# Kernel tuning notes

Hardware: AMD Instinct MI355X
Metric: run time of the kernel (lower is better)

The kernel has to match this reference:

```python
import jax, jax.numpy as jnp
import numpy as np

B, N, DEG = 8, 4096, 16
E = N * DEG            # edges per graph
IN, HID, C, OUT = 128, 512, 2, 10
EPS = 1e-15


def setup_inputs() -> dict:
    key = jax.random.key(0)
    ks = jax.random.split(key, 16)
    # within-graph random edges, then offset each graph by b*N
    src = jax.random.randint(ks[0], (B, E), 0, N)
    dst = jax.random.randint(ks[1], (B, E), 0, N)
    off = (jnp.arange(B) * N)[:, None]
    edge_index = jnp.stack([(src + off).reshape(-1), (dst + off).reshape(-1)], axis=0).astype(jnp.int64)
    batch = jnp.repeat(jnp.arange(B), N).astype(jnp.int64)
    x = jax.random.normal(ks[2], (B * N, IN), dtype=jnp.float32)
    edge_weight = jax.random.uniform(ks[3], (B * E,), dtype=jnp.float32)
    g = lambda k, s: (0.02 * jax.random.normal(k, s, dtype=jnp.float32))
    return {
        "x": x, "edge_index": edge_index, "batch": batch, "edge_weight": edge_weight,
        "W_rel1": g(ks[4], (IN, HID)), "b_rel1": jnp.zeros((HID,), jnp.float32),
        "W_root1": g(ks[5], (IN, HID)),
        "W_pool": g(ks[6], (HID, C)), "b_pool": jnp.zeros((C,), jnp.float32),
        "W_rel3": g(ks[7], (HID, HID)), "b_rel3": jnp.zeros((HID,), jnp.float32),
        "W_root3": g(ks[8], (HID, HID)),
        "W_lin1": g(ks[9], (HID, HID)), "b_lin1": jnp.zeros((HID,), jnp.float32),
        "W_lin2": g(ks[10], (HID, OUT)), "b_lin2": jnp.zeros((OUT,), jnp.float32),
    }


def reference(x, edge_index, batch, edge_weight,
              W_rel1, b_rel1, W_root1, W_pool, b_pool,
              W_rel3, b_rel3, W_root3, W_lin1, b_lin1, W_lin2, b_lin2):
    src, dst = edge_index[0], edge_index[1]
    # GraphConv (aggr='add'): out = lin_rel(sum_j w_ji x_j) + lin_root(x)
    agg = jax.ops.segment_sum(x[src] * edge_weight[:, None], dst, num_segments=B * N)
    h = jax.nn.relu(agg @ W_rel1 + b_rel1 + x @ W_root1)          # [BN, HID]
    s_logits = h @ W_pool + b_pool                                 # [BN, C]

    # dense batched tensors (equal-size graphs)
    hd = h.reshape(B, N, HID)
    s = jax.nn.softmax(s_logits.reshape(B, N, C), axis=-1)
    b_idx = batch[src]
    r = src - b_idx * N
    c = dst - b_idx * N
    adj = jnp.zeros((B, N, N), jnp.float32).at[b_idx, r, c].add(edge_weight)

    # dense mincut pooling
    out = jnp.einsum('bnc,bnf->bcf', s, hd)                        # [B, C, HID]
    sA = jnp.einsum('bnc,bnm->bcm', s, adj)
    out_adj = jnp.einsum('bcm,bmk->bck', sA, s)                    # [B, C, C]
    mincut_num = jnp.einsum('bcc->b', out_adj)
    d = adj.sum(-1)                                                # [B, N]
    mincut_den = jnp.einsum('bnc,bn,bnc->b', s, d, s)
    mc_loss = jnp.mean(-(mincut_num / mincut_den))
    ss = jnp.einsum('bnc,bnk->bck', s, s)
    ss_n = ss / jnp.linalg.norm(ss, axis=(1, 2), keepdims=True)
    i_s = jnp.eye(C, dtype=jnp.float32) / jnp.sqrt(jnp.float32(C))
    o_loss = jnp.mean(jnp.linalg.norm(ss_n - i_s[None], axis=(1, 2)))
    # zero diagonal + symmetric degree normalization
    out_adj = out_adj * (1.0 - jnp.eye(C, dtype=jnp.float32))[None]
    d2 = jnp.sqrt(out_adj.sum(-1)) + EPS                           # [B, C]
    out_adj = out_adj / d2[:, :, None] / d2[:, None, :]

    # conv3 on pooled graph: edges (row->col) of dense adj => agg = A^T x
    agg3 = jnp.einsum('bij,bif->bjf', out_adj, out)
    x3 = agg3 @ W_rel3 + b_rel3 + out @ W_root3                    # [B, C, HID]
    xm = x3.mean(axis=1)                                           # [B, HID]
    h2 = jax.nn.relu(xm @ W_lin1 + b_lin1)
    logits = h2 @ W_lin2 + b_lin2
    return (jax.nn.log_softmax(logits, axis=-1), mc_loss, o_loss, s_logits, out_adj)
```

## Files before the change

kernel.cpp:

```cpp
#include <hip/hip_runtime.h>
#include <hip/hip_bf16.h>

#define BB 8
#define NN 4096
#define EE 65536
#define BE (BB*EE)
#define BN (BB*NN)
#define INF 128
#define HID 512
#define CC 2
#define OUTC 10
#define ELLCAP 64

typedef __bf16 bf16x8_t __attribute__((ext_vector_type(8)));
typedef float  f32x4_t  __attribute__((ext_vector_type(4)));

__device__ __forceinline__ ushort f2bf(float f) {
  union { float f; unsigned u; } v; v.f = f;
  unsigned r = v.u + 0x7FFFu + ((v.u >> 16) & 1u);
  return (ushort)(r >> 16);
}
__device__ __forceinline__ float bf2f(ushort s) {
  union { unsigned u; float f; } v; v.u = ((unsigned)s) << 16;
  return v.f;
}

__global__ __launch_bounds__(256) void front(
    const int* __restrict__ src, const int* __restrict__ dst,
    const float* __restrict__ ew, const float* __restrict__ x,
    const float* __restrict__ Wrel, const float* __restrict__ Wroot,
    int* __restrict__ deg, int2* __restrict__ ell,
    ushort* __restrict__ Ab, ushort* __restrict__ Bb) {
  int blk = blockIdx.x;
  int tid = threadIdx.x;
  if (blk < 4096) {
    int g = (blk & 7) * 131072 + (blk >> 3) * 256 + tid;
    float4 v = *(const float4*)&x[(size_t)g * 4];
    int m = g >> 5;
    int kin = (g & 31) * 4;
    ushort4 o;
    o.x = f2bf(v.x); o.y = f2bf(v.y); o.z = f2bf(v.z); o.w = f2bf(v.w);
    *(ushort4*)&Ab[(size_t)m * 256 + 128 + kin] = o;
  } else if (blk < 6144) {
    int bl = blk - 4096;
    int e = (bl & 7) * EE + (bl >> 3) * 256 + tid;
    int d = dst[e];
    int p = atomicAdd(&deg[d], 1);
    if (p < ELLCAP) {
      int2 v; v.x = src[e]; v.y = __float_as_int(ew[e]);
      ell[(size_t)d * ELLCAP + p] = v;
    }
  } else {
    int g = (blk - 6144) * 256 + tid;
    int n = g & 511, k = g >> 9;
    float w = (k < 128) ? Wrel[k * 512 + n] : Wroot[(k - 128) * 512 + n];
    Bb[n * 256 + k] = f2bf(w);
  }
}

__global__ __launch_bounds__(256) void gather_ell(
    const int* __restrict__ deg, const int2* __restrict__ ell,
    ushort* __restrict__ Ab) {
  int blk = blockIdx.x;
  int n = (blk & 7) * NN + (blk >> 3) * 4 + (threadIdx.x >> 6);
  int lane = threadIdx.x & 63;
  int l4 = lane >> 4;
  int fl = lane & 15;
  int d = deg[n]; if (d > ELLCAP) d = ELLCAP;
  const int2* ep = ell + (size_t)n * ELLCAP;

  float a[8] = {0, 0, 0, 0, 0, 0, 0, 0};
  int j = 0;
  for (; j + 7 < d; j += 8) {
    int2 v0 = ep[j + l4];
    int2 v1 = ep[j + 4 + l4];
    uint4 u0 = *(const uint4*)&Ab[(size_t)v0.x * 256 + 128 + fl * 8];
    uint4 u1 = *(const uint4*)&Ab[(size_t)v1.x * 256 + 128 + fl * 8];
    float w0 = __int_as_float(v0.y);
    float w1 = __int_as_float(v1.y);
    const ushort* s0 = (const ushort*)&u0;
    const ushort* s1 = (const ushort*)&u1;
#pragma unroll
    for (int q = 0; q < 8; ++q)
      a[q] += w0 * bf2f(s0[q]) + w1 * bf2f(s1[q]);
  }
  for (; j + 3 < d; j += 4) {
    int2 v0 = ep[j + l4];
    uint4 u0 = *(const uint4*)&Ab[(size_t)v0.x * 256 + 128 + fl * 8];
    float w0 = __int_as_float(v0.y);
    const ushort* s0 = (const ushort*)&u0;
#pragma unroll
    for (int q = 0; q < 8; ++q)
      a[q] += w0 * bf2f(s0[q]);
  }
  {
    int idx = j + l4;
    if (idx < d) {
      int2 v0 = ep[idx];
      uint4 u0 = *(const uint4*)&Ab[(size_t)v0.x * 256 + 128 + fl * 8];
      float w0 = __int_as_float(v0.y);
      const ushort* s0 = (const ushort*)&u0;
#pragma unroll
      for (int q = 0; q < 8; ++q)
        a[q] += w0 * bf2f(s0[q]);
    }
  }
#pragma unroll
  for (int q = 0; q < 8; ++q) {
    a[q] += __shfl_xor(a[q], 16, 64);
    a[q] += __shfl_xor(a[q], 32, 64);
  }
  if (l4 == 0) {
    ushort o[8];
#pragma unroll
    for (int q = 0; q < 8; ++q) o[q] = f2bf(a[q]);
    *(uint4*)&Ab[(size_t)n * 256 + fl * 8] = *(const uint4*)o;
  }
}

__global__ __launch_bounds__(256) void gemm_pool(
    const ushort* __restrict__ Ab, const ushort* __restrict__ Bb,
    const float* __restrict__ brel, const float* __restrict__ Wp,
    const float* __restrict__ bp, float* __restrict__ s,
    float* __restrict__ slog, float* __restrict__ outpart,
    float* __restrict__ ssacc) {
  __shared__ ushort As[64 * 256];
  __shared__ ushort Bs[64 * 256];
  __shared__ float wpS[1024];
  __shared__ float brS[512];
  __shared__ float2 ssv[64];
  __shared__ float ssrw[16][3];
  __shared__ float oacc[1024];
  int tid = threadIdx.x;
  int blk = blockIdx.x;
  int b = blk & 7;
  int chunk = blk >> 3;
  int m0 = b * NN + chunk * 64;
  int obik = b * 64 + chunk;

#pragma unroll
  for (int i = 0; i < 8; ++i) {
    int g = tid + i * 256;
    int r = g >> 5, c = g & 31;
    int cs = c ^ (r & 31);
    *(uint4*)&As[(r * 32 + cs) * 8] = *(const uint4*)&Ab[(size_t)(m0 + r) * 256 + c * 8];
  }
  *(float4*)&wpS[tid * 4] = *(const float4*)&Wp[tid * 4];
  if (tid < 128) *(float4*)&brS[tid * 4] = *(const float4*)&brel[tid * 4];
  *(float4*)&oacc[tid * 4] = (float4){0.f, 0.f, 0.f, 0.f};

  int wave = tid >> 6, lane = tid & 63;
  int wm = wave * 16;
  int l16 = lane & 15, quad = lane >> 4;
  int arow = wm + l16;
  float bp0 = bp[0], bp1 = bp[1];

  float la0[4] = {0, 0, 0, 0}, la1[4] = {0, 0, 0, 0};
  uint hpk[8][4][2];

  for (int cc = 0; cc < 8; ++cc) {
    int n0 = cc * 64;
#pragma unroll
    for (int i = 0; i < 8; ++i) {
      int g = tid + i * 256;
      int r = g >> 5, c = g & 31;
      int cs = c ^ (r & 31);
      *(uint4*)&Bs[(r * 32 + cs) * 8] = *(const uint4*)&Bb[(size_t)(n0 + r) * 256 + c * 8];
    }
    __syncthreads();

    f32x4_t acc[4];
#pragma unroll
    for (int ct = 0; ct < 4; ++ct) acc[ct] = (f32x4_t){0.f, 0.f, 0.f, 0.f};
#pragma unroll
    for (int kc = 0; kc < 8; ++kc) {
      int cl = kc * 4 + quad;
      bf16x8_t af = *(const bf16x8_t*)&As[(arow * 32 + (cl ^ (arow & 31))) * 8];
#pragma unroll
      for (int ct = 0; ct < 4; ++ct) {
        int brow = ct * 16 + l16;
        bf16x8_t bf = *(const bf16x8_t*)&Bs[(brow * 32 + (cl ^ (brow & 31))) * 8];
        acc[ct] = __builtin_amdgcn_mfma_f32_16x16x32_bf16(af, bf, acc[ct], 0, 0, 0);
      }
    }
#pragma unroll
    for (int ct = 0; ct < 4; ++ct) {
      int col = cc * 64 + ct * 16 + l16;
      float bias = brS[col];
      float w0 = wpS[col * 2], w1 = wpS[col * 2 + 1];
      float h0 = fmaxf(acc[ct][0] + bias, 0.f);
      float h1 = fmaxf(acc[ct][1] + bias, 0.f);
      float h2 = fmaxf(acc[ct][2] + bias, 0.f);
      float h3 = fmaxf(acc[ct][3] + bias, 0.f);
      la0[0] += h0 * w0; la1[0] += h0 * w1;
      la0[1] += h1 * w0; la1[1] += h1 * w1;
      la0[2] += h2 * w0; la1[2] += h2 * w1;
      la0[3] += h3 * w0; la1[3] += h3 * w1;
      hpk[cc][ct][0] = (uint)f2bf(h0) | ((uint)f2bf(h1) << 16);
      hpk[cc][ct][1] = (uint)f2bf(h2) | ((uint)f2bf(h3) << 16);
    }
    __syncthreads();
  }

#pragma unroll
  for (int r = 0; r < 4; ++r) {
#pragma unroll
    for (int m = 1; m < 16; m <<= 1) {
      la0[r] += __shfl_xor(la0[r], m, 64);
      la1[r] += __shfl_xor(la1[r], m, 64);
    }
  }
  if (l16 == 0) {
    float sa = 0.f, sb = 0.f, sc2 = 0.f;
#pragma unroll
    for (int r = 0; r < 4; ++r) {
      int row = wm + quad * 4 + r;
      int n = m0 + row;
      float l0 = la0[r] + bp0, l1 = la1[r] + bp1;
      slog[n * 2] = l0;
      slog[n * 2 + 1] = l1;
      float mm = fmaxf(l0, l1);
      float e0 = expf(l0 - mm), e1 = expf(l1 - mm);
      float inv = 1.f / (e0 + e1);
      float s0 = e0 * inv, s1 = e1 * inv;
      *(float2*)&s[n * 2] = make_float2(s0, s1);
      ssv[row] = make_float2(s0, s1);
      sa += s0 * s0; sb += s0 * s1; sc2 += s1 * s1;
    }
    int idx = wave * 4 + quad;
    ssrw[idx][0] = sa; ssrw[idx][1] = sb; ssrw[idx][2] = sc2;
  }
  __syncthreads();

  {
    float2 sv0 = ssv[wm + quad * 4 + 0];
    float2 sv1 = ssv[wm + quad * 4 + 1];
    float2 sv2 = ssv[wm + quad * 4 + 2];
    float2 sv3 = ssv[wm + quad * 4 + 3];
#pragma unroll
    for (int cc = 0; cc < 8; ++cc) {
#pragma unroll
      for (int ct = 0; ct < 4; ++ct) {
        int col = cc * 64 + ct * 16 + l16;
        uint p0 = hpk[cc][ct][0];
        uint p1 = hpk[cc][ct][1];
        float h0 = bf2f((ushort)(p0 & 0xFFFFu));
        float h1 = bf2f((ushort)(p0 >> 16));
        float h2 = bf2f((ushort)(p1 & 0xFFFFu));
        float h3 = bf2f((ushort)(p1 >> 16));
        float v0 = sv0.x * h0 + sv1.x * h1 + sv2.x * h2 + sv3.x * h3;
        float v1 = sv0.y * h0 + sv1.y * h1 + sv2.y * h2 + sv3.y * h3;
        v0 += __shfl_xor(v0, 16, 64); v0 += __shfl_xor(v0, 32, 64);
        v1 += __shfl_xor(v1, 16, 64); v1 += __shfl_xor(v1, 32, 64);
        if (lane < 16) {
          atomicAdd(&oacc[col], v0);
          atomicAdd(&oacc[512 + col], v1);
        }
      }
    }
  }
  __syncthreads();

#pragma unroll
  for (int q = 0; q < 4; ++q) {
    int idx = tid + q * 256;
    outpart[(size_t)obik * 1024 + idx] = oacc[idx];
  }
  if (tid < 3) {
    float v = 0.f;
#pragma unroll
    for (int i = 0; i < 16; ++i) v += ssrw[i][tid];
    atomicAdd(&ssacc[b * 4 + tid], v);
  }
}

__global__ __launch_bounds__(256) void edge_pass2(
    const int* __restrict__ src, const int* __restrict__ dst,
    const float* __restrict__ ew, const float* __restrict__ s,
    float* __restrict__ oadj, float* __restrict__ mden) {
  int b = blockIdx.x & 7;
  int sub = blockIdx.x >> 3;
  int base = b * EE + sub * 1024;
  float p00 = 0, p01 = 0, p10 = 0, p11 = 0, md = 0;
  for (int i = threadIdx.x; i < 1024; i += 256) {
    int e = base + i;
    int r = src[e], c = dst[e];
    float w = ew[e];
    float s0r = s[r * 2], s1r = s[r * 2 + 1];
    float s0c = s[c * 2], s1c = s[c * 2 + 1];
    p00 += w * s0r * s0c; p01 += w * s0r * s1c;
    p10 += w * s1r * s0c; p11 += w * s1r * s1c;
    md  += w * (s0r * s0r + s1r * s1r);
  }
#pragma unroll
  for (int off = 32; off; off >>= 1) {
    p00 += __shfl_down(p00, off, 64);
    p01 += __shfl_down(p01, off, 64);
    p10 += __shfl_down(p10, off, 64);
    p11 += __shfl_down(p11, off, 64);
    md  += __shfl_down(md,  off, 64);
  }
  __shared__ float red[4][5];
  int wave = threadIdx.x >> 6, lane = threadIdx.x & 63;
  if (lane == 0) {
    red[wave][0] = p00; red[wave][1] = p01;
    red[wave][2] = p10; red[wave][3] = p11;
    red[wave][4] = md;
  }
  __syncthreads();
  if (threadIdx.x < 4) {
    float v = red[0][threadIdx.x] + red[1][threadIdx.x] +
              red[2][threadIdx.x] + red[3][threadIdx.x];
    atomicAdd(&oadj[b * 4 + threadIdx.x], v);
  } else if (threadIdx.x == 4) {
    float v = red[0][4] + red[1][4] + red[2][4] + red[3][4];
    atomicAdd(&mden[b], v);
  }
}

__global__ __launch_bounds__(256) void finalize_a(
    const float* __restrict__ outpart, const float* __restrict__ oadj,
    const float* __restrict__ ssacc, const float* __restrict__ mden,
    float* __restrict__ uv, float* __restrict__ lossp,
    float* __restrict__ dout) {
  __shared__ float sc[2];
  __shared__ float r0[256], r1[256];
  int b = blockIdx.x >> 3, fc = blockIdx.x & 7;
  int t = threadIdx.x;
  if (t == 0) {
    float r00 = oadj[b * 4 + 0], r01 = oadj[b * 4 + 1];
    float r10 = oadj[b * 4 + 2], r11 = oadj[b * 4 + 3];
    float d20 = sqrtf(r01) + 1e-15f;
    float d21 = sqrtf(r10) + 1e-15f;
    float oa01 = r01 / (d20 * d21);
    float oa10 = r10 / (d21 * d20);
    sc[0] = oa01; sc[1] = oa10;
    if (fc == 0) {
      lossp[b * 2 + 0] = -((r00 + r11) / mden[b]) / (float)BB;
      float a = ssacc[b * 4 + 0], bb = ssacc[b * 4 + 1], c = ssacc[b * 4 + 2];
      float nrm = sqrtf(a * a + 2.f * bb * bb + c * c);
      float q = 0.70710678118654752f;
      float da = a / nrm - q, db = bb / nrm, dc = c / nrm - q;
      lossp[b * 2 + 1] = sqrtf(da * da + 2.f * db * db + dc * dc) / (float)BB;
      dout[65618 + b * 4 + 0] = 0.f;
      dout[65618 + b * 4 + 1] = oa01;
      dout[65618 + b * 4 + 2] = oa10;
      dout[65618 + b * 4 + 3] = 0.f;
    }
  }
  __syncthreads();
  int f = fc * 64 + (t & 63);
  int ic = t >> 6;
  float o0s = 0.f, o1s = 0.f;
  for (int i = ic * 16; i < ic * 16 + 16; ++i) {
    o0s += outpart[(size_t)(b * 64 + i) * 1024 + f];
    o1s += outpart[(size_t)(b * 64 + i) * 1024 + 512 + f];
  }
  r0[ic * 64 + (t & 63)] = o0s;
  r1[ic * 64 + (t & 63)] = o1s;
  __syncthreads();
  if (ic == 0) {
    int fl = t & 63;
    float a0 = r0[fl] + r0[64 + fl] + r0[128 + fl] + r0[192 + fl];
    float a1 = r1[fl] + r1[64 + fl] + r1[128 + fl] + r1[192 + fl];
    uv[b * HID + f] = sc[1] * a1 + sc[0] * a0;
    uv[BB * HID + b * HID + f] = a0 + a1;
  }
}

__global__ __launch_bounds__(256) void conv3_part(
    const float* __restrict__ uv, const float* __restrict__ Wrel3,
    const float* __restrict__ Wroot3, float* __restrict__ xmacc) {
  __shared__ float us[8][32], vs[8][32];
  __shared__ float red[4][64][8];
  int blk = blockIdx.x;
  int fc = blk & 7, kc = blk >> 3;
  int t = threadIdx.x;
  {
    int b = t >> 5, k = t & 31;
    us[b][k] = uv[b * HID + kc * 32 + k];
    vs[b][k] = uv[BB * HID + b * HID + kc * 32 + k];
  }
  __syncthreads();
  int f = fc * 64 + (t & 63);
  int ks = t >> 6;
  float acc[8] = {0, 0, 0, 0, 0, 0, 0, 0};
#pragma unroll
  for (int j = 0; j < 8; ++j) {
    int kl = ks * 8 + j;
    int k = kc * 32 + kl;
    float wr = Wrel3[k * HID + f];
    float wo = Wroot3[k * HID + f];
#pragma unroll
    for (int b = 0; b < 8; ++b)
      acc[b] += us[b][kl] * wr + vs[b][kl] * wo;
  }
#pragma unroll
  for (int b = 0; b < 8; ++b) red[ks][t & 63][b] = acc[b];
  __syncthreads();
  if (ks == 0) {
    int fl = t & 63;
#pragma unroll
    for (int b = 0; b < 8; ++b) {
      float v = red[0][fl][b] + red[1][fl][b] + red[2][fl][b] + red[3][fl][b];
      atomicAdd(&xmacc[b * HID + f], v);
    }
  }
}

__global__ __launch_bounds__(256) void lin1_part(
    const float* __restrict__ xmacc, const float* __restrict__ brel3,
    const float* __restrict__ Wlin1, float* __restrict__ h2acc) {
  __shared__ float xs[8][32];
  __shared__ float red[4][64][8];
  int blk = blockIdx.x;
  int fc = blk & 7, kc = blk >> 3;
  int t = threadIdx.x;
  {
    int b = t >> 5, k = t & 31;
    xs[b][k] = 0.5f * xmacc[b * HID + kc * 32 + k] + brel3[kc * 32 + k];
  }
  __syncthreads();
  int f = fc * 64 + (t & 63);
  int ks = t >> 6;
  float acc[8] = {0, 0, 0, 0, 0, 0, 0, 0};
#pragma unroll
  for (int j = 0; j < 8; ++j) {
    int kl = ks * 8 + j;
    int k = kc * 32 + kl;
    float w = Wlin1[k * HID + f];
#pragma unroll
    for (int b = 0; b < 8; ++b)
      acc[b] += xs[b][kl] * w;
  }
#pragma unroll
  for (int b = 0; b < 8; ++b) red[ks][t & 63][b] = acc[b];
  __syncthreads();
  if (ks == 0) {
    int fl = t & 63;
#pragma unroll
    for (int b = 0; b < 8; ++b) {
      float v = red[0][fl][b] + red[1][fl][b] + red[2][fl][b] + red[3][fl][b];
      atomicAdd(&h2acc[b * HID + f], v);
    }
  }
}

__global__ __launch_bounds__(256) void head(
    const float* __restrict__ h2acc, const float* __restrict__ blin1,
    const float* __restrict__ Wlin2, const float* __restrict__ blin2,
    const float* __restrict__ lossp, float* __restrict__ dout) {
  __shared__ float hs[HID];
  __shared__ float lg[16];
  __shared__ float lse;
  int b = blockIdx.x, t = threadIdx.x;
  if (b == 0 && t == 255) {
    float l0 = 0.f, l1 = 0.f;
#pragma unroll
    for (int i = 0; i < BB; ++i) { l0 += lossp[i * 2]; l1 += lossp[i * 2 + 1]; }
    dout[80] = l0;
    dout[81] = l1;
  }
  for (int i = t; i < HID; i += 256)
    hs[i] = fmaxf(h2acc[b * HID + i] + blin1[i], 0.f);
  __syncthreads();
  int wave = t >> 6, lane = t & 63;
  for (int o = wave; o < OUTC; o += 4) {
    float acc = 0.f;
    for (int k = lane; k < HID; k += 64)
      acc += hs[k] * Wlin2[k * OUTC + o];
#pragma unroll
    for (int off = 32; off; off >>= 1) acc += __shfl_down(acc, off, 64);
    if (lane == 0) lg[o] = acc + blin2[o];
  }
  __syncthreads();
  if (t == 0) {
    float m = lg[0];
    for (int o = 1; o < OUTC; ++o) m = fmaxf(m, lg[o]);
    float se = 0.f;
    for (int o = 0; o < OUTC; ++o) se += expf(lg[o] - m);
    lse = m + logf(se);
  }
  __syncthreads();
  if (t < OUTC) dout[b * OUTC + t] = lg[t] - lse;
}

extern "C" void kernel_launch(void* const* d_in, const int* in_sizes, int n_in,
                              void* d_out, int out_size, void* d_ws, size_t ws_size,
                              hipStream_t stream) {
  const float* x      = (const float*)d_in[0];
  const int*   ei     = (const int*)d_in[1];
  const float* ew     = (const float*)d_in[3];
  const float* Wrel1  = (const float*)d_in[4];
  const float* brel1  = (const float*)d_in[5];
  const float* Wroot1 = (const float*)d_in[6];
  const float* Wpool  = (const float*)d_in[7];
  const float* bpool  = (const float*)d_in[8];
  const float* Wrel3  = (const float*)d_in[9];
  const float* brel3  = (const float*)d_in[10];
  const float* Wroot3 = (const float*)d_in[11];
  const float* Wlin1  = (const float*)d_in[12];
  const float* blin1  = (const float*)d_in[13];
  const float* Wlin2  = (const float*)d_in[14];
  const float* blin2  = (const float*)d_in[15];
  float* out = (float*)d_out;
  float* ws  = (float*)d_ws;

  float* oadj  = ws + 40960;
  float* ssacc = oadj + 32;
  float* mden  = ssacc + 32;
  int*   deg   = (int*)(mden + 8);
  float* xmacc = ws + 73800;
  float* h2acc = xmacc + 4096;
  float* lossp = ws + 81992;
  ushort* Ab   = (ushort*)(ws + 106568);
  ushort* Bb   = (ushort*)(ws + 4300872);
  float* outpart = ws + 12763208;
  float* s     = ws + 16000000;
  int2*  ell   = (int2*)(ws + 4366408);
  float* uv    = (float*)deg;

  const int* src = ei;
  const int* dst = ei + BE;

  hipMemsetAsync(ws + 40960, 0, (size_t)41032 * sizeof(float), stream);

  front      <<<6656, 256, 0, stream>>>(src, dst, ew, x, Wrel1, Wroot1,
                                        deg, ell, Ab, Bb);
  gather_ell <<<BN / 4, 256, 0, stream>>>(deg, ell, Ab);
  gemm_pool  <<<512, 256, 0, stream>>>(Ab, Bb, brel1, Wpool, bpool,
                                       s, out + 82, outpart, ssacc);
  edge_pass2 <<<BB * 64, 256, 0, stream>>>(src, dst, ew, s, oadj, mden);
  finalize_a <<<64, 256, 0, stream>>>(outpart, oadj, ssacc, mden, uv, lossp, out);
  conv3_part <<<128, 256, 0, stream>>>(uv, Wrel3, Wroot3, xmacc);
  lin1_part  <<<128, 256, 0, stream>>>(xmacc, brel3, Wlin1, h2acc);
  head       <<<BB, 256, 0, stream>>>(h2acc, blin1, Wlin2, blin2, lossp, out);
}
```

Measured before the change: 230.1 us.

## Spill h tile to global bf16 buffer instead of registers for pooling reduction

The GEMM epilogue no longer keeps all 64 packed h values per thread in registers. Each 64x64 h tile is staged through shared memory and written to a global bf16 buffer. The S^T·H reduction then rereads each wave's 16 rows from global memory and writes per-wave partials with no shared-memory atomics, and finalize_a now sums four times as many partials. This lowers register pressure and drops the LDS atomics, at the cost of extra global traffic, a reread of h, and a larger partial reduction.

New measurement: 213.8 us. -7.1%, faster.

```diff
diff --git a/kernel.cpp b/kernel.cpp
--- a/kernel.cpp
+++ b/kernel.cpp
@@ -121,16 +121,15 @@
 __global__ __launch_bounds__(256) void gemm_pool(
     const ushort* __restrict__ Ab, const ushort* __restrict__ Bb,
     const float* __restrict__ brel, const float* __restrict__ Wp,
-    const float* __restrict__ bp, float* __restrict__ s,
-    float* __restrict__ slog, float* __restrict__ outpart,
-    float* __restrict__ ssacc) {
+    const float* __restrict__ bp, ushort* __restrict__ hbf,
+    float* __restrict__ s, float* __restrict__ slog,
+    float* __restrict__ outpart, float* __restrict__ ssacc) {
   __shared__ ushort As[64 * 256];
   __shared__ ushort Bs[64 * 256];
-  __shared__ float wpS[1024];
+  __shared__ ushort hC[64 * 72];
   __shared__ float brS[512];
   __shared__ float2 ssv[64];
   __shared__ float ssrw[16][3];
-  __shared__ float oacc[1024];
   int tid = threadIdx.x;
   int blk = blockIdx.x;
   int b = blk & 7;
@@ -145,9 +144,7 @@
     int cs = c ^ (r & 31);
     *(uint4*)&As[(r * 32 + cs) * 8] = *(const uint4*)&Ab[(size_t)(m0 + r) * 256 + c * 8];
   }
-  *(float4*)&wpS[tid * 4] = *(const float4*)&Wp[tid * 4];
   if (tid < 128) *(float4*)&brS[tid * 4] = *(const float4*)&brel[tid * 4];
-  *(float4*)&oacc[tid * 4] = (float4){0.f, 0.f, 0.f, 0.f};
 
   int wave = tid >> 6, lane = tid & 63;
   int wm = wave * 16;
@@ -156,7 +153,6 @@
   float bp0 = bp[0], bp1 = bp[1];
 
   float la0[4] = {0, 0, 0, 0}, la1[4] = {0, 0, 0, 0};
-  uint hpk[8][4][2];
 
   for (int cc = 0; cc < 8; ++cc) {
     int n0 = cc * 64;
@@ -185,9 +181,10 @@
     }
 #pragma unroll
     for (int ct = 0; ct < 4; ++ct) {
-      int col = cc * 64 + ct * 16 + l16;
+      int col = n0 + ct * 16 + l16;
       float bias = brS[col];
-      float w0 = wpS[col * 2], w1 = wpS[col * 2 + 1];
+      float w0 = Wp[col * 2], w1 = Wp[col * 2 + 1];
+      int rowb = wm + quad * 4;
       float h0 = fmaxf(acc[ct][0] + bias, 0.f);
       float h1 = fmaxf(acc[ct][1] + bias, 0.f);
       float h2 = fmaxf(acc[ct][2] + bias, 0.f);
@@ -196,10 +193,20 @@
       la0[1] += h1 * w0; la1[1] += h1 * w1;
       la0[2] += h2 * w0; la1[2] += h2 * w1;
       la0[3] += h3 * w0; la1[3] += h3 * w1;
-      hpk[cc][ct][0] = (uint)f2bf(h0) | ((uint)f2bf(h1) << 16);
-      hpk[cc][ct][1] = (uint)f2bf(h2) | ((uint)f2bf(h3) << 16);
+      int cbase = ct * 16 + l16;
+      hC[(rowb + 0) * 72 + cbase] = f2bf(h0);
+      hC[(rowb + 1) * 72 + cbase] = f2bf(h1);
+      hC[(rowb + 2) * 72 + cbase] = f2bf(h2);
+      hC[(rowb + 3) * 72 + cbase] = f2bf(h3);
     }
     __syncthreads();
+    {
+      int r = tid >> 2, co = (tid & 3) * 16;
+      uint4 v0 = *(uint4*)&hC[r * 72 + co];
+      uint4 v1 = *(uint4*)&hC[r * 72 + co + 8];
+      *(uint4*)&hbf[(size_t)(m0 + r) * 512 + n0 + co] = v0;
+      *(uint4*)&hbf[(size_t)(m0 + r) * 512 + n0 + co + 8] = v1;
+    }
   }
 
 #pragma unroll
@@ -233,38 +240,26 @@
   __syncthreads();
 
   {
-    float2 sv0 = ssv[wm + quad * 4 + 0];
-    float2 sv1 = ssv[wm + quad * 4 + 1];
-    float2 sv2 = ssv[wm + quad * 4 + 2];
-    float2 sv3 = ssv[wm + quad * 4 + 3];
-#pragma unroll
-    for (int cc = 0; cc < 8; ++cc) {
-#pragma unroll
-      for (int ct = 0; ct < 4; ++ct) {
-        int col = cc * 64 + ct * 16 + l16;
-        uint p0 = hpk[cc][ct][0];
-        uint p1 = hpk[cc][ct][1];
-        float h0 = bf2f((ushort)(p0 & 0xFFFFu));
-        float h1 = bf2f((ushort)(p0 >> 16));
-        float h2 = bf2f((ushort)(p1 & 0xFFFFu));
-        float h3 = bf2f((ushort)(p1 >> 16));
-        float v0 = sv0.x * h0 + sv1.x * h1 + sv2.x * h2 + sv3.x * h3;
-        float v1 = sv0.y * h0 + sv1.y * h1 + sv2.y * h2 + sv3.y * h3;
-        v0 += __shfl_xor(v0, 16, 64); v0 += __shfl_xor(v0, 32, 64);
-        v1 += __shfl_xor(v1, 16, 64); v1 += __shfl_xor(v1, 32, 64);
-        if (lane < 16) {
-          atomicAdd(&oacc[col], v0);
-          atomicAdd(&oacc[512 + col], v1);
-        }
+    int f0 = lane * 8;
+    float o0[8] = {0, 0, 0, 0, 0, 0, 0, 0};
+    float o1[8] = {0, 0, 0, 0, 0, 0, 0, 0};
+    for (int i = 0; i < 16; ++i) {
+      int row = wm + i;
+      float2 sv = ssv[row];
+      bf16x8_t hv = *(const bf16x8_t*)&hbf[(size_t)(m0 + row) * 512 + f0];
+      const ushort* hp = (const ushort*)&hv;
+#pragma unroll
+      for (int j = 0; j < 8; ++j) {
+        float h = bf2f(hp[j]);
+        o0[j] += sv.x * h;
+        o1[j] += sv.y * h;
       }
     }
-  }
-  __syncthreads();
-
-#pragma unroll
-  for (int q = 0; q < 4; ++q) {
-    int idx = tid + q * 256;
-    outpart[(size_t)obik * 1024 + idx] = oacc[idx];
+    size_t base = (size_t)(obik * 4 + wave) * 1024;
+    *(float4*)&outpart[base + f0]       = *(float4*)&o0[0];
+    *(float4*)&outpart[base + f0 + 4]   = *(float4*)&o0[4];
+    *(float4*)&outpart[base + 512 + f0]     = *(float4*)&o1[0];
+    *(float4*)&outpart[base + 512 + f0 + 4] = *(float4*)&o1[4];
   }
   if (tid < 3) {
     float v = 0.f;
@@ -352,9 +347,9 @@
   int f = fc * 64 + (t & 63);
   int ic = t >> 6;
   float o0s = 0.f, o1s = 0.f;
-  for (int i = ic * 16; i < ic * 16 + 16; ++i) {
-    o0s += outpart[(size_t)(b * 64 + i) * 1024 + f];
-    o1s += outpart[(size_t)(b * 64 + i) * 1024 + 512 + f];
+  for (int i = ic * 64; i < ic * 64 + 64; ++i) {
+    o0s += outpart[(size_t)(b * 256 + i) * 1024 + f];
+    o1s += outpart[(size_t)(b * 256 + i) * 1024 + 512 + f];
   }
   r0[ic * 64 + (t & 63)] = o0s;
   r1[ic * 64 + (t & 63)] = o1s;
@@ -515,6 +510,7 @@
   float* lossp = ws + 81992;
   ushort* Ab   = (ushort*)(ws + 106568);
   ushort* Bb   = (ushort*)(ws + 4300872);
+  ushort* hbf  = (ushort*)(ws + 4366408);
   float* outpart = ws + 12763208;
   float* s     = ws + 16000000;
   int2*  ell   = (int2*)(ws + 4366408);
@@ -528,7 +524,7 @@
   front      <<<6656, 256, 0, stream>>>(src, dst, ew, x, Wrel1, Wroot1,
                                         deg, ell, Ab, Bb);
   gather_ell <<<BN / 4, 256, 0, stream>>>(deg, ell, Ab);
-  gemm_pool  <<<512, 256, 0, stream>>>(Ab, Bb, brel1, Wpool, bpool,
+  gemm_pool  <<<512, 256, 0, stream>>>(Ab, Bb, brel1, Wpool, bpool, hbf,
                                        s, out + 82, outpart, ssacc);
   edge_pass2 <<<BB * 64, 256, 0, stream>>>(src, dst, ew, s, oadj, mden);
   finalize_a <<<64, 256, 0, stream>>>(outpart, oadj, ssacc, mden, uv, lossp, out);
```
